# Kernel tuning notes

Measured on AMD Instinct MI355X. Metric: run time of the kernel, lower is better.

## Reference

```python
import jax, jax.numpy as jnp
import numpy as np
from jax import lax

V, H, B, S, NSLOT, T, G, NSW = 20000, 400, 16, 256, 30, 10, 3, 40


def setup_inputs() -> dict:
    key = jax.random.key(0)
    ks = jax.random.split(key, 24)
    p = lambda k, shape: jax.random.normal(k, shape, dtype=jnp.float32) * 0.1
    return {
        'story': jax.random.randint(ks[0], (B, S), 0, V),
        'enc_lens': jax.random.randint(ks[1], (B,), S // 2, S + 1),
        'target_batches': jax.random.randint(ks[2], (B, NSLOT, T), 0, V),
        'domain_idx': jax.random.randint(ks[3], (NSLOT,), 0, NSW),
        'slot_idx': jax.random.randint(ks[4], (NSLOT,), 0, NSW),
        'emb': p(ks[5], (V, H)),
        'enc_Wih_f': p(ks[6], (3 * H, H)), 'enc_Whh_f': p(ks[7], (3 * H, H)),
        'enc_bih_f': p(ks[8], (3 * H,)), 'enc_bhh_f': p(ks[9], (3 * H,)),
        'enc_Wih_b': p(ks[10], (3 * H, H)), 'enc_Whh_b': p(ks[11], (3 * H, H)),
        'enc_bih_b': p(ks[12], (3 * H,)), 'enc_bhh_b': p(ks[13], (3 * H,)),
        'dec_Wih': p(ks[14], (3 * H, H)), 'dec_Whh': p(ks[15], (3 * H, H)),
        'dec_bih': p(ks[16], (3 * H,)), 'dec_bhh': p(ks[17], (3 * H,)),
        'Wr': p(ks[18], (1, 3 * H)), 'br': p(ks[19], (1,)),
        'Wg': p(ks[20], (G, H)), 'bg': p(ks[21], (G,)),
        'slot_table': p(ks[22], (NSW, H)),
    }


def _gru_scan(x, m, h0, Wih, Whh, bih, bhh):
    # x: [S,B,H], m: [S,B] validity mask (packed-sequence semantics)
    def step(h, xm):
        xt, mt = xm
        gi = xt @ Wih.T + bih
        gh = h @ Whh.T + bhh
        ir, iz, inn = jnp.split(gi, 3, -1)
        hr, hz, hn = jnp.split(gh, 3, -1)
        r = jax.nn.sigmoid(ir + hr)
        z = jax.nn.sigmoid(iz + hz)
        n = jnp.tanh(inn + r * hn)
        hnew = (1.0 - z) * n + z * h
        h = jnp.where(mt[:, None], hnew, h)
        y = jnp.where(mt[:, None], hnew, 0.0)
        return h, y
    hT, ys = lax.scan(step, h0, (x, m))
    return ys, hT


def reference(story, enc_lens, target_batches, domain_idx, slot_idx, emb,
              enc_Wih_f, enc_Whh_f, enc_bih_f, enc_bhh_f,
              enc_Wih_b, enc_Whh_b, enc_bih_b, enc_bhh_b,
              dec_Wih, dec_Whh, dec_bih, dec_bhh,
              Wr, br, Wg, bg, slot_table):
    Bc, Sc = story.shape
    nslot = domain_idx.shape[0]
    Tc = target_batches.shape[2]
    NB = nslot * Bc

    # ----- EncoderRNN: bidirectional GRU over story (seq-major) -----
    x = emb[story.T]                                   # [S,B,H]
    mask = jnp.arange(Sc)[:, None] < enc_lens[None, :]  # [S,B]
    h0 = jnp.zeros((Bc, H), jnp.float32)
    ys_f, h_f = _gru_scan(x, mask, h0, enc_Wih_f, enc_Whh_f, enc_bih_f, enc_bhh_f)
    ys_b, h_b = _gru_scan(x[::-1], mask[::-1], h0, enc_Wih_b, enc_Whh_b, enc_bih_b, enc_bhh_b)
    ys_b = ys_b[::-1]
    encoded_outputs = (ys_f + ys_b).transpose(1, 0, 2)  # [B,S,H]
    enc_hidden = h_f + h_b                              # [B,H]

    # ----- Generator (parallel decode, teacher forcing) -----
    combined = slot_table[domain_idx] + slot_table[slot_idx]           # [nslot,H]
    slot_emb_arr = jnp.repeat(combined[:, None, :], Bc, axis=1).reshape(NB, H)
    hidden0 = jnp.tile(enc_hidden, (nslot, 1))                         # [NB,H]
    enc_out = jnp.tile(encoded_outputs, (nslot, 1, 1))                 # [NB,S,H]
    lens_rep = jnp.tile(enc_lens, nslot)
    story_rep = jnp.tile(story, (nslot, 1))                            # [NB,S]
    attn_mask = jnp.arange(Sc)[None, :] < lens_rep[:, None]            # [NB,S]
    rows = jnp.arange(NB)[:, None]

    # teacher-forced decoder inputs: step0 = slot emb, then gold tokens
    tgt_flat = target_batches.transpose(1, 0, 2).reshape(NB, Tc)       # [NB,T]
    dec_in = jnp.concatenate([slot_emb_arr[None], emb[tgt_flat[:, :Tc - 1].T]], axis=0)  # [T,NB,H]

    def dec_step(h, x_in):
        gi = x_in @ dec_Wih.T + dec_bih
        gh = h @ dec_Whh.T + dec_bhh
        ir, iz, inn = jnp.split(gi, 3, -1)
        hr, hz, hn = jnp.split(gh, 3, -1)
        r = jax.nn.sigmoid(ir + hr)
        z = jax.nn.sigmoid(iz + hz)
        n = jnp.tanh(inn + r * hn)
        h = (1.0 - z) * n + z * h                      # dec_state == new hidden
        scores = jnp.einsum('nh,nsh->ns', h, enc_out)
        scores = jnp.where(attn_mask, scores, -jnp.inf)
        prob = jax.nn.softmax(scores, axis=1)          # [NB,S]
        context = jnp.einsum('ns,nsh->nh', prob, enc_out)
        p_vocab = jax.nn.softmax(h @ emb.T, axis=1)    # [NB,V]
        p_gen_vec = jnp.concatenate([h, context, x_in], axis=-1)
        sw = jax.nn.sigmoid(p_gen_vec @ Wr.T + br)     # [NB,1]
        p_ctx = jnp.zeros_like(p_vocab).at[rows, story_rep].add(prob)
        final_p = (1.0 - sw) * p_ctx + sw * p_vocab
        return h, (final_p, context)

    _, (finals, contexts) = lax.scan(dec_step, hidden0, dec_in)
    all_point_outputs = finals.reshape(Tc, nslot, Bc, V).transpose(1, 2, 0, 3)  # [nslot,B,T,V]
    all_gate_outputs = (contexts[0] @ Wg.T + bg).reshape(nslot, Bc, G)
    return all_point_outputs, all_gate_outputs
```

## Files before the change

kernel.cpp:

```cpp
#include <hip/hip_runtime.h>
#include <hip/hip_bf16.h>

typedef unsigned short u16;
typedef __attribute__((ext_vector_type(8))) short bf16x8;
typedef __attribute__((ext_vector_type(4))) float f32x4;
typedef __attribute__((ext_vector_type(4))) unsigned u32x4;

static constexpr int V = 20000, H = 400, B = 16, S = 256, NSLOT = 30, T = 10, G = 3;
static constexpr int H3 = 3 * H;
static constexpr int NB = NSLOT * B;
static constexpr int ENBLK = 20;
static constexpr int ESL   = 20;
static constexpr int EROWS = 64;
static constexpr int EKP   = 416;
static constexpr int HP2 = 424;
static constexpr int SCP = 260;
static constexpr int PP  = 264;
static constexpr int CXP = 404;
static constexpr int FUSED_LDS = 32*HP2*2 + 32*SCP*4 + 32*PP*2 + 32*CXP*4;

__device__ __forceinline__ float bf2f(u16 v) {
    union { unsigned u; float f; } x; x.u = ((unsigned)v) << 16; return x.f;
}
__device__ __forceinline__ u16 f2bf(float f) {
    union { float f; unsigned u; } x; x.f = f;
    unsigned r = x.u + 0x7fffu + ((x.u >> 16) & 1u);
    return (u16)(r >> 16);
}
__device__ __forceinline__ float sigm(float v) { return 1.f / (1.f + __expf(-v)); }

__global__ __launch_bounds__(256) void gemm_bt(
    const u16* __restrict__ A, const u16* __restrict__ Bt,
    const float* __restrict__ bias, float* __restrict__ C,
    int M, int N, int K, int lda, int ldb, long long ldc,
    long long sA, long long sB, long long sC,
    int mode, float* __restrict__ rowsum)
{
    __shared__ u16 As[64][40];
    __shared__ u16 Bs[64][40];
    const int bz = blockIdx.z;
    A  += (long long)bz * sA;
    Bt += (long long)bz * sB;
    C  += (long long)bz * sC;
    const int m0 = blockIdx.x * 64, n0 = blockIdx.y * 64;
    const int tid = threadIdx.x, wave = tid >> 6, lane = tid & 63;
    const int wm = (wave >> 1) * 32, wn = (wave & 1) * 32;
    const int srow = tid >> 2, scol = (tid & 3) * 8;
// ... 77 lines not shown
                float s = acc[i][0][r] + acc[i][1][r];
                s += __shfl_xor(s, 1); s += __shfl_xor(s, 2);
                s += __shfl_xor(s, 4); s += __shfl_xor(s, 8);
                if (fr == 0) {
                    int row = m0 + wm + i * 16 + kq * 4 + r;
                    if (row < M) atomicAdd(&rowsum[row], s);
                }
            }
    }
}

__global__ void cvt_bf16_kernel(const float* __restrict__ src, u16* __restrict__ dst, int n) {
    for (int i = blockIdx.x * blockDim.x + threadIdx.x; i < n; i += gridDim.x * blockDim.x)
        dst[i] = f2bf(src[i]);
}

__global__ void cvt4_kernel(const float* __restrict__ a, const float* __restrict__ b,
                            const float* __restrict__ c, const float* __restrict__ d,
                            u16* __restrict__ da, u16* __restrict__ db,
                            u16* __restrict__ dc, u16* __restrict__ dd, int n) {
    for (int i = blockIdx.x * blockDim.x + threadIdx.x; i < n; i += gridDim.x * blockDim.x) {
        da[i] = f2bf(a[i]); db[i] = f2bf(b[i]); dc[i] = f2bf(c[i]); dd[i] = f2bf(d[i]);
    }
}

__global__ void prep_wenc_kernel(const float* __restrict__ whhf, const float* __restrict__ whhb,
                                 u16* __restrict__ dst) {
    int idx = blockIdx.x * 256 + threadIdx.x;
    const int total = 2 * ENBLK * EROWS * EKP;
    if (idx >= total) return;
    int k = idx % EKP; int r = idx / EKP;
    int rloc = r % EROWS; r /= EROWS;
    int j = r % ENBLK; int dir = r / ENBLK;
    u16 v = 0;
    if (k < H && rloc < 3 * ESL) {
        int g = rloc / ESL, c = rloc % ESL;
        const float* W = dir ? whhb : whhf;
        v = f2bf(W[(long long)(g * H + j * ESL + c) * H + k]);
    }
    dst[idx] = v;
}

__global__ void embed_story_kernel(const int* __restrict__ story, const u16* __restrict__ embb,
                                   u16* __restrict__ xb) {
    int row = blockIdx.x;
    int s = row >> 4, b = row & 15;
    int tok = story[b * S + s];
    const u16* e = embb + (long long)tok * H;
    u16* d = xb + (long long)row * H;
    for (int k = threadIdx.x; k < H; k += blockDim.x) d[k] = e[k];
}

__global__ void build_decin_kernel(const int* __restrict__ tgt, const int* __restrict__ dom,
                                   const int* __restrict__ sidx, const float* __restrict__ slt,
                                   const u16* __restrict__ embb, u16* __restrict__ decin) {
    int n = blockIdx.x, t = blockIdx.y;
    int b = n & 15, slot = n >> 4;
    u16* d = decin + ((long long)t * NB + n) * H;
    if (t == 0) {
        const float* s1 = slt + (long long)dom[slot] * H;
        const float* s2 = slt + (long long)sidx[slot] * H;
        for (int k = threadIdx.x; k < H; k += blockDim.x) d[k] = f2bf(s1[k] + s2[k]);
    } else {
        int tok = tgt[(b * NSLOT + slot) * T + (t - 1)];
        const u16* e = embb + (long long)tok * H;
        for (int k = threadIdx.x; k < H; k += blockDim.x) d[k] = e[k];
    }
}

__global__ __launch_bounds__(256) void enc_rnn2_kernel(
    const u16* __restrict__ wencp,
    const float* __restrict__ bhhf, const float* __restrict__ bhhb,
    const float* __restrict__ gif, const float* __restrict__ gib,
    const int* __restrict__ lens,
    unsigned* __restrict__ hbuf, int* __restrict__ flags,
    float* __restrict__ ysf, float* __restrict__ ysb,
    float* __restrict__ hfo, float* __restrict__ hbo)
{
    const int bid = blockIdx.x;
    const int dir = bid / ENBLK, j = bid % ENBLK;
    const float* bhh = dir ? bhhb : bhhf;
    const float* gi  = dir ? gib  : gif;
    float* ys = dir ? ysb : ysf;
    float* ho = dir ? hbo : hfo;

    __shared__ u16 wlds[EROWS * EKP];
    __shared__ float ghs[EROWS * 17];

    const int tid = threadIdx.x, wave = tid >> 6, lane = tid & 63;
    const int fr = lane & 15, kq = lane >> 4;

    const u16* wsrc = wencp + (long long)(dir * ENBLK + j) * EROWS * EKP;
    for (int i = tid * 8; i < EROWS * EKP; i += 256 * 8)
        *(bf16x8*)&wlds[i] = *(const bf16x8*)&wsrc[i];
    for (int i = tid; i < EROWS * 17; i += 256) ghs[i] = 0.f;

    const int p0 = tid, p1 = 256 + tid;
    const bool has1 = (tid < 64);
    const int b0 = p0 / ESL, kl0 = p0 % ESL;
    const int b1 = has1 ? p1 / ESL : 0, kl1 = has1 ? p1 % ESL : 0;
    const int k0 = j * ESL;
    const int len0 = lens[b0];
    const int len1 = has1 ? lens[b1] : 0;
    const float bhr0 = bhh[k0 + kl0], bhz0 = bhh[H + k0 + kl0], bhn0 = bhh[2 * H + k0 + kl0];
    const float bhr1 = has1 ? bhh[k0 + kl1] : 0.f;
    const float bhz1 = has1 ? bhh[H + k0 + kl1] : 0.f;
    const float bhn1 = has1 ? bhh[2 * H + k0 + kl1] : 0.f;
    float h0r = 0.f, h1r = 0.f;

    unsigned* hb_d = hbuf + (long long)dir * S * B * EKP;
    int* flg_d = flags + dir * S * ENBLK;
    const u16* arow = &wlds[(wave * 16 + fr) * EKP + kq * 8];
    __syncthreads();

    for (int t = 0; t < S; ++t) {
        const int s = dir ? (S - 1 - t) : t;
        const float* gbase = gi + (long long)s * B * H3;
        float gr0 = gbase[b0 * H3 + k0 + kl0];
        float gz0 = gbase[b0 * H3 + H + k0 + kl0];
        float gn0 = gbase[b0 * H3 + 2 * H + k0 + kl0];
        float gr1 = 0.f, gz1 = 0.f, gn1 = 0.f;
        if (has1) {
            gr1 = gbase[b1 * H3 + k0 + kl1];
            gz1 = gbase[b1 * H3 + H + k0 + kl1];
            gn1 = gbase[b1 * H3 + 2 * H + k0 + kl1];
        }

        f32x4 acc = (f32x4){0.f, 0.f, 0.f, 0.f};
        if (t > 0) {
            const int* fl = flg_d + (t - 1) * ENBLK;
            for (;;) {
                int v = 1;
                if (lane < ENBLK)
                    v = __hip_atomic_load(&fl[lane], __ATOMIC_RELAXED,
                                          __HIP_MEMORY_SCOPE_AGENT);
                if (__all(v != 0)) break;
                __builtin_amdgcn_s_sleep(2);
            }
            asm volatile("" ::: "memory");
            const unsigned* hrow = hb_d + ((long long)(t - 1) * B + fr) * EKP + kq * 8;
            f32x4 acch = (f32x4){0.f, 0.f, 0.f, 0.f};
            f32x4 accl = (f32x4){0.f, 0.f, 0.f, 0.f};
#pragma unroll
            for (int kk = 0; kk < 13; ++kk) {
                u32x4 a = *(const u32x4*)(hrow + kk * 32);
                u32x4 b = *(const u32x4*)(hrow + kk * 32 + 4);
                union { unsigned u[4]; bf16x8 v; } hi, lo;
                hi.u[0] = __builtin_amdgcn_perm(a[1], a[0], 0x05040100u);
                hi.u[1] = __builtin_amdgcn_perm(a[3], a[2], 0x05040100u);
                hi.u[2] = __builtin_amdgcn_perm(b[1], b[0], 0x05040100u);
                hi.u[3] = __builtin_amdgcn_perm(b[3], b[2], 0x05040100u);
                lo.u[0] = __builtin_amdgcn_perm(a[1], a[0], 0x07060302u);
                lo.u[1] = __builtin_amdgcn_perm(a[3], a[2], 0x07060302u);
                lo.u[2] = __builtin_amdgcn_perm(b[1], b[0], 0x07060302u);
                lo.u[3] = __builtin_amdgcn_perm(b[3], b[2], 0x07060302u);
                bf16x8 av = *(const bf16x8*)(arow + kk * 32);
                acch = __builtin_amdgcn_mfma_f32_16x16x32_bf16(av, hi.v, acch, 0, 0, 0);
                accl = __builtin_amdgcn_mfma_f32_16x16x32_bf16(av, lo.v, accl, 0, 0, 0);
            }
            acc = acch + accl;
        }
#pragma unroll
        for (int r = 0; r < 4; ++r) ghs[(wave * 16 + kq * 4 + r) * 17 + fr] = acc[r];
        __syncthreads();

        unsigned* hpub = hb_d + (long long)t * B * EKP;
        {
            float ghr = ghs[kl0 * 17 + b0];
            float ghz = ghs[(ESL + kl0) * 17 + b0];
            float ghn = ghs[(2 * ESL + kl0) * 17 + b0];
            float rg = sigm(gr0 + ghr + bhr0);
            float zg = sigm(gz0 + ghz + bhz0);
            float ng = tanhf(gn0 + rg * (ghn + bhn0));
            float hn = (1.f - zg) * ng + zg * h0r;
            bool msk = s < len0;
            float y = msk ? hn : 0.f;
            if (msk) h0r = hn;
            ys[((long long)(b0 * S + s)) * H + k0 + kl0] = y;
            u16 hi = f2bf(h0r);
            unsigned packed = (unsigned)hi | ((unsigned)f2bf(h0r - bf2f(hi)) << 16);
            __hip_atomic_store(&hpub[b0 * EKP + k0 + kl0], packed, __ATOMIC_RELAXED,
                               __HIP_MEMORY_SCOPE_AGENT);
        }
        if (has1) {
            float ghr = ghs[kl1 * 17 + b1];
            float ghz = ghs[(ESL + kl1) * 17 + b1];
            float ghn = ghs[(2 * ESL + kl1) * 17 + b1];
            float rg = sigm(gr1 + ghr + bhr1);
            float zg = sigm(gz1 + ghz + bhz1);
            float ng = tanhf(gn1 + rg * (ghn + bhn1));
            float hn = (1.f - zg) * ng + zg * h1r;
            bool msk = s < len1;
            float y = msk ? hn : 0.f;
            if (msk) h1r = hn;
            ys[((long long)(b1 * S + s)) * H + k0 + kl1] = y;
            u16 hi = f2bf(h1r);
            unsigned packed = (unsigned)hi | ((unsigned)f2bf(h1r - bf2f(hi)) << 16);
            __hip_atomic_store(&hpub[b1 * EKP + k0 + kl1], packed, __ATOMIC_RELAXED,
                               __HIP_MEMORY_SCOPE_AGENT);
        }
        __syncthreads();
        if (tid == 0)
            __hip_atomic_store(&flg_d[t * ENBLK + j], 1, __ATOMIC_RELAXED,
                               __HIP_MEMORY_SCOPE_AGENT);
    }
    ho[b0 * H + k0 + kl0] = h0r;
    if (has1) ho[b1 * H + k0 + kl1] = h1r;
}

__global__ void packE_kernel(const float* __restrict__ ysf, const float* __restrict__ ysb,
                             u16* __restrict__ E, u16* __restrict__ ET) {
    __shared__ u16 tile[32][400];
    const int b = blockIdx.x, s0 = blockIdx.y * 32;
    for (int si = 0; si < 32; ++si) {
        const long long base = ((long long)b * S + s0 + si) * H;
        for (int k = threadIdx.x; k < H; k += blockDim.x) {
            u16 v = f2bf(ysf[base + k] + ysb[base + k]);
            E[base + k] = v;
            tile[si][k] = v;
        }
    }
    __syncthreads();
    for (int idx = threadIdx.x; idx < 32 * H; idx += blockDim.x) {
        int k = idx >> 5, si = idx & 31;
        ET[((long long)b * H + k) * S + s0 + si] = tile[si][k];
    }
}

__global__ void h0_kernel(const float* __restrict__ hf, const float* __restrict__ hb,
                          float* __restrict__ hf32, u16* __restrict__ hnk) {
    int n = blockIdx.x, b = n & 15;
    for (int k = threadIdx.x; k < H; k += blockDim.x) {
        float v = hf[b * H + k] + hb[b * H + k];
        hf32[(long long)n * H + k] = v;
        hnk[(long long)n * H + k] = f2bf(v);
    }
}

__global__ __launch_bounds__(512) void fused_step_kernel(
    const float* __restrict__ dgi, const float* __restrict__ dgh,
    float* __restrict__ hf32, u16* __restrict__ hall,
    const u16* __restrict__ decinb,
    const u16* __restrict__ Eb, const u16* __restrict__ ETb,
    const int* __restrict__ lens,
    const float* __restrict__ Wr, const float* __restrict__ br,
    const float* __restrict__ Wg, const float* __restrict__ bg,
    float* __restrict__ probfT, float* __restrict__ swvT,
    float* __restrict__ gout, int t)
{
    extern __shared__ char smem[];
    u16*   hls = (u16*)smem;
    float* scs = (float*)(smem + 32 * HP2 * 2);
    u16*   pls = (u16*)(smem + 32 * HP2 * 2 + 32 * SCP * 4);
    float* cxs = (float*)(smem + 32 * HP2 * 2 + 32 * SCP * 4 + 32 * PP * 2);

    const int b = blockIdx.x;
    const int tid = threadIdx.x, wave = tid >> 6, lane = tid & 63;
    const int fr = lane & 15, kq = lane >> 4;
    const int len = lens[b];

    for (int i = tid; i < 32 * (HP2 - H); i += 512) {
        int r = i / (HP2 - H), c = H + i % (HP2 - H);
        hls[r * HP2 + c] = 0;
    }
    for (int i = tid; i < 2 * HP2; i += 512) hls[30 * HP2 + i] = 0;
    for (int i = tid; i < 2 * PP; i += 512) pls[30 * PP + i] = 0;

    for (int i = tid; i < 30 * H; i += 512) {
        int slot = i / H, k = i % H;
        int n = slot * 16 + b;
        const float* gi = dgi + ((long long)t * NB + n) * H3;
        const float* gh = dgh + (long long)n * H3;
        float r  = sigm(gi[k] + gh[k]);
        float z  = sigm(gi[H + k] + gh[H + k]);
        float nn = tanhf(gi[2 * H + k] + r * gh[2 * H + k]);
        float h  = hf32[(long long)n * H + k];
        float hn = (1.f - z) * nn + z * h;
        hf32[(long long)n * H + k] = hn;
        u16 hb = f2bf(hn);
        hall[((long long)t * NB + n) * H + k] = hb;
        hls[slot * HP2 + k] = hb;
    }
    __syncthreads();

    {
        const int nt0 = wave * 2;
        f32x4 acc[2][2];
#pragma unroll
        for (int i = 0; i < 2; ++i)
#pragma unroll
            for (int jj = 0; jj < 2; ++jj) acc[i][jj] = (f32x4){0.f, 0.f, 0.f, 0.f};
        const u16* br0 = Eb + ((long long)b * S + nt0 * 16 + fr) * H + kq * 8;
        const u16* br1 = Eb + ((long long)b * S + (nt0 + 1) * 16 + fr) * H + kq * 8;
        const u16* ar0 = hls + fr * HP2 + kq * 8;
        const u16* ar1 = hls + (16 + fr) * HP2 + kq * 8;
#pragma unroll
        for (int kk = 0; kk < 13; ++kk) {
            bf16x8 av0 = *(const bf16x8*)(ar0 + kk * 32);
            bf16x8 av1 = *(const bf16x8*)(ar1 + kk * 32);
            bf16x8 bv0, bv1;
            if (kk == 12 && kq >= 2) {
                bv0 = (bf16x8){0,0,0,0,0,0,0,0}; bv1 = bv0;
            } else {
                bv0 = *(const bf16x8*)(br0 + kk * 32);
                bv1 = *(const bf16x8*)(br1 + kk * 32);
            }
            acc[0][0] = __builtin_amdgcn_mfma_f32_16x16x32_bf16(av0, bv0, acc[0][0], 0, 0, 0);
            acc[1][0] = __builtin_amdgcn_mfma_f32_16x16x32_bf16(av1, bv0, acc[1][0], 0, 0, 0);
            acc[0][1] = __builtin_amdgcn_mfma_f32_16x16x32_bf16(av0, bv1, acc[0][1], 0, 0, 0);
            acc[1][1] = __builtin_amdgcn_mfma_f32_16x16x32_bf16(av1, bv1, acc[1][1], 0, 0, 0);
        }
#pragma unroll
        for (int i = 0; i < 2; ++i)
#pragma unroll
            for (int jj = 0; jj < 2; ++jj)
#pragma unroll
                for (int r = 0; r < 4; ++r)
                    scs[(i * 16 + kq * 4 + r) * SCP + (nt0 + jj) * 16 + fr] = acc[i][jj][r];
    }
    __syncthreads();

    for (int i = 0; i < 4; ++i) {
        int row = wave * 4 + i;
        if (row >= 30) break;
        int n = row * 16 + b;
        float v[4];
        float mx = -3.0e38f;
#pragma unroll
        for (int q = 0; q < 4; ++q) {
            int s = lane + 64 * q;
            float x = (s < len) ? scs[row * SCP + s] : -3.0e38f;
            v[q] = x; mx = fmaxf(mx, x);
        }
        mx = fmaxf(mx, __shfl_xor(mx, 1));  mx = fmaxf(mx, __shfl_xor(mx, 2));
        mx = fmaxf(mx, __shfl_xor(mx, 4));  mx = fmaxf(mx, __shfl_xor(mx, 8));
        mx = fmaxf(mx, __shfl_xor(mx, 16)); mx = fmaxf(mx, __shfl_xor(mx, 32));
        float sum = 0.f;
#pragma unroll
        for (int q = 0; q < 4; ++q) {
            int s = lane + 64 * q;
            float e = (s < len) ? __expf(v[q] - mx) : 0.f;
            v[q] = e; sum += e;
        }
        sum += __shfl_xor(sum, 1);  sum += __shfl_xor(sum, 2);
        sum += __shfl_xor(sum, 4);  sum += __shfl_xor(sum, 8);
        sum += __shfl_xor(sum, 16); sum += __shfl_xor(sum, 32);
        float inv = 1.f / sum;
#pragma unroll
        for (int q = 0; q < 4; ++q) {
            int s = lane + 64 * q;
            float pr = v[q] * inv;
            pls[row * PP + s] = f2bf(pr);
            probfT[((long long)(t * NB + n)) * S + s] = pr;
        }
    }
    __syncthreads();

    for (int nt = wave; nt < 25; nt += 8) {
        f32x4 acc0 = (f32x4){0.f,0.f,0.f,0.f}, acc1 = (f32x4){0.f,0.f,0.f,0.f};
        const u16* brow = ETb + ((long long)b * H + nt * 16 + fr) * S + kq * 8;
        const u16* ar0 = pls + fr * PP + kq * 8;
        const u16* ar1 = pls + (16 + fr) * PP + kq * 8;
#pragma unroll
        for (int kk = 0; kk < 8; ++kk) {
            bf16x8 bv  = *(const bf16x8*)(brow + kk * 32);
            bf16x8 av0 = *(const bf16x8*)(ar0 + kk * 32);
            bf16x8 av1 = *(const bf16x8*)(ar1 + kk * 32);
            acc0 = __builtin_amdgcn_mfma_f32_16x16x32_bf16(av0, bv, acc0, 0, 0, 0);
            acc1 = __builtin_amdgcn_mfma_f32_16x16x32_bf16(av1, bv, acc1, 0, 0, 0);
        }
#pragma unroll
        for (int r = 0; r < 4; ++r) {
            cxs[(kq * 4 + r) * CXP + nt * 16 + fr] = acc0[r];
            cxs[(16 + kq * 4 + r) * CXP + nt * 16 + fr] = acc1[r];
        }
    }
    __syncthreads();

    for (int i = 0; i < 4; ++i) {
        int slot = wave + 8 * i;
        if (slot >= 30) break;
        int n = slot * 16 + b;
        const u16* xrow = decinb + ((long long)t * NB + n) * H;
        float p = 0.f;
        for (int k = lane; k < H; k += 64)
            p += bf2f(hls[slot * HP2 + k]) * Wr[k]
               + cxs[slot * CXP + k] * Wr[H + k]
               + bf2f(xrow[k]) * Wr[2 * H + k];
        p += __shfl_xor(p, 1);  p += __shfl_xor(p, 2);
        p += __shfl_xor(p, 4);  p += __shfl_xor(p, 8);
        p += __shfl_xor(p, 16); p += __shfl_xor(p, 32);
        if (lane == 0) swvT[t * NB + n] = sigm(p + br[0]);
        if (t == 0) {
            for (int g = 0; g < G; ++g) {
                float q = 0.f;
                for (int k = lane; k < H; k += 64)
                    q += cxs[slot * CXP + k] * Wg[g * H + k];
                q += __shfl_xor(q, 1);  q += __shfl_xor(q, 2);
                q += __shfl_xor(q, 4);  q += __shfl_xor(q, 8);
                q += __shfl_xor(q, 16); q += __shfl_xor(q, 32);
                if (lane == 0) gout[(long long)n * G + g] = q + bg[g];
            }
        }
    }
}

__global__ void scale_all_kernel(float* __restrict__ out, const float* __restrict__ swvT,
                                 const float* __restrict__ rowsumT) {
    const int n = blockIdx.x;
    const int col = blockIdx.y * 256 + threadIdx.x;
    if (col >= V) return;
#pragma unroll
    for (int t = 0; t < T; ++t) {
        float f = swvT[t * NB + n] / rowsumT[t * NB + n];
        out[((long long)n * T + t) * V + col] *= f;
    }
}

__global__ void scatter_all_kernel(float* __restrict__ out, const int* __restrict__ story,
                                   const int* __restrict__ lens, const float* __restrict__ swvT,
                                   const float* __restrict__ probfT) {
    const int n = blockIdx.x, t = blockIdx.y, b = n & 15, s = threadIdx.x;
    if (s < lens[b]) {
        int tok = story[b * S + s];
        atomicAdd(out + ((long long)n * T + t) * V + tok,
                  (1.f - swvT[t * NB + n]) * probfT[((long long)(t * NB + n)) * S + s]);
    }
}

extern "C" void kernel_launch(void* const* d_in, const int* in_sizes, int n_in,
                              void* d_out, int out_size, void* d_ws, size_t ws_size,
                              hipStream_t stream) {
    const int*   story = (const int*)d_in[0];
    const int*   lens  = (const int*)d_in[1];
    const int*   tgt   = (const int*)d_in[2];
    const int*   dom   = (const int*)d_in[3];
// ... 2 lines not shown
    const float* wihf  = (const float*)d_in[6];
    const float* whhf  = (const float*)d_in[7];
    const float* bihf  = (const float*)d_in[8];
    const float* bhhf  = (const float*)d_in[9];
    const float* wihb  = (const float*)d_in[10];
    const float* whhb  = (const float*)d_in[11];
    const float* bihb  = (const float*)d_in[12];
    const float* bhhb  = (const float*)d_in[13];
    const float* dwih  = (const float*)d_in[14];
    const float* dwhh  = (const float*)d_in[15];
    const float* dbih  = (const float*)d_in[16];
    const float* dbhh  = (const float*)d_in[17];
    const float* Wr    = (const float*)d_in[18];
    const float* br    = (const float*)d_in[19];
    const float* Wg    = (const float*)d_in[20];
    const float* bg    = (const float*)d_in[21];
    const float* slt   = (const float*)d_in[22];
    float* out = (float*)d_out;

    char* wsb = (char*)d_ws;
    size_t off = 0;
    auto alloc = [&](size_t bytes) -> char* {
        char* p = wsb + off;
        off += (bytes + 255) & ~(size_t)255;
        return p;
    };
    u16*   embb   = (u16*)alloc((size_t)V * H * 2);
    u16*   wihfb  = (u16*)alloc((size_t)H3 * H * 2);
    u16*   wihbb  = (u16*)alloc((size_t)H3 * H * 2);
    u16*   dwihb  = (u16*)alloc((size_t)H3 * H * 2);
    u16*   dwhhb  = (u16*)alloc((size_t)H3 * H * 2);
    u16*   wencp  = (u16*)alloc((size_t)2 * ENBLK * EROWS * EKP * 2);
    unsigned* hbuf = (unsigned*)alloc((size_t)2 * S * B * EKP * 4);
    int*   flags  = (int*)alloc((size_t)2 * S * ENBLK * 4);
    u16*   xb     = (u16*)alloc((size_t)S * B * H * 2);
    u16*   decinb = (u16*)alloc((size_t)T * NB * H * 2);
    float* gif    = (float*)alloc((size_t)S * B * H3 * 4);
    float* gib    = (float*)alloc((size_t)S * B * H3 * 4);
    float* dgi    = (float*)alloc((size_t)T * NB * H3 * 4);
    float* ysf    = (float*)alloc((size_t)B * S * H * 4);
    float* ysb    = (float*)alloc((size_t)B * S * H * 4);
    float* hfv    = (float*)alloc((size_t)B * H * 4);
    float* hbv    = (float*)alloc((size_t)B * H * 4);
    u16*   Eb     = (u16*)alloc((size_t)B * S * H * 2);
    u16*   ETb    = (u16*)alloc((size_t)B * H * S * 2);
    float* hf32   = (float*)alloc((size_t)NB * H * 4);
    u16*   hnk    = (u16*)alloc((size_t)NB * H * 2);
    u16*   hall   = (u16*)alloc((size_t)T * NB * H * 2);
    float* dgh    = (float*)alloc((size_t)NB * H3 * 4);
    float* probfT = (float*)alloc((size_t)T * NB * S * 4);
    float* swvT   = (float*)alloc((size_t)T * NB * 4);
    float* rowsumT = (float*)alloc((size_t)T * NB * 4);
    (void)ws_size; (void)in_sizes; (void)n_in; (void)out_size;

    auto launch_gemm = [&](const u16* A, const u16* Bt, const float* bias, float* C,
                           int M, int N, int K, int lda, int ldb, long long ldc,
                           long long sA, long long sB, long long sC, int nb,
                           int mode, float* rs) {
        dim3 g((M + 63) / 64, (N + 63) / 64, nb);
        gemm_bt<<<g, 256, 0, stream>>>(A, Bt, bias, C, M, N, K, lda, ldb, ldc,
                                       sA, sB, sC, mode, rs);
    };

    hipFuncSetAttribute((const void*)fused_step_kernel,
                        hipFuncAttributeMaxDynamicSharedMemorySize, FUSED_LDS);

    cvt_bf16_kernel<<<2048, 256, 0, stream>>>(emb, embb, V * H);
    cvt4_kernel<<<1024, 256, 0, stream>>>(wihf, wihb, dwih, dwhh,
                                          wihfb, wihbb, dwihb, dwhhb, H3 * H);
    {
        const int total = 2 * ENBLK * EROWS * EKP;
        prep_wenc_kernel<<<(total + 255) / 256, 256, 0, stream>>>(whhf, whhb, wencp);
    }
    embed_story_kernel<<<S * B, 256, 0, stream>>>(story, embb, xb);
    { dim3 g(NB, T); build_decin_kernel<<<g, 256, 0, stream>>>(tgt, dom, sidx, slt, embb, decinb); }

    launch_gemm(xb, wihfb, bihf, gif, S * B, H3, H, H, H, H3, 0, 0, 0, 1, 0, nullptr);
    launch_gemm(xb, wihbb, bihb, gib, S * B, H3, H, H, H, H3, 0, 0, 0, 1, 0, nullptr);
    launch_gemm(decinb, dwihb, dbih, dgi, T * NB, H3, H, H, H, H3, 0, 0, 0, 1, 0, nullptr);

    hipMemsetAsync(flags, 0, (size_t)2 * S * ENBLK * 4, stream);
    hipMemsetAsync(hbuf, 0, (size_t)2 * S * B * EKP * 4, stream);
    hipMemsetAsync(rowsumT, 0, (size_t)T * NB * 4, stream);
    enc_rnn2_kernel<<<2 * ENBLK, 256, 0, stream>>>(wencp, bhhf, bhhb, gif, gib, lens,
                                                   hbuf, flags, ysf, ysb, hfv, hbv);
    { dim3 g(B, S / 32); packE_kernel<<<g, 256, 0, stream>>>(ysf, ysb, Eb, ETb); }
    h0_kernel<<<NB, 256, 0, stream>>>(hfv, hbv, hf32, hnk);

    for (int t = 0; t < T; ++t) {
        const u16* hprev = (t == 0) ? hnk : hall + (size_t)(t - 1) * NB * H;
        launch_gemm(hprev, dwhhb, dbhh, dgh, NB, H3, H, H, H, H3, 0, 0, 0, 1, 0, nullptr);
        fused_step_kernel<<<16, 512, FUSED_LDS, stream>>>(
            dgi, dgh, hf32, hall, decinb, Eb, ETb, lens, Wr, br, Wg, bg,
            probfT, swvT, out + (size_t)NB * T * V, t);
    }

    launch_gemm(hall, embb, nullptr, out, T * NB, V, H, H, H, V,
                0, 0, 0, 1, 2, rowsumT);
    { dim3 g(NB, (V + 255) / 256); scale_all_kernel<<<g, 256, 0, stream>>>(out, swvT, rowsumT); }
    { dim3 g(NB, T); scatter_all_kernel<<<g, 256, 0, stream>>>(out, story, lens, swvT, probfT); }
}
```

Before: 2.473 ms.

## Make encoder GRU waves independent with per-wave flags instead of block barriers

```diff
diff --git a/kernel.cpp b/kernel.cpp
--- a/kernel.cpp
+++ b/kernel.cpp
@@ -13,6 +13,7 @@
 static constexpr int ESL   = 20;
 static constexpr int EROWS = 64;
 static constexpr int EKP   = 416;
+static constexpr int NFLG  = 4 * ENBLK;
 static constexpr int HP2 = 424;
 static constexpr int SCP = 260;
 static constexpr int PP  = 264;
@@ -156,11 +157,12 @@
     int k = idx % EKP; int r = idx / EKP;
     int rloc = r % EROWS; r /= EROWS;
     int j = r % ENBLK; int dir = r / ENBLK;
+    int w = rloc >> 4, m = rloc & 15;
     u16 v = 0;
-    if (k < H && rloc < 3 * ESL) {
-        int g = rloc / ESL, c = rloc % ESL;
+    if (k < H && m < 15) {
+        int g = m / 5, cc = m % 5;
         const float* W = dir ? whhb : whhf;
-        v = f2bf(W[(long long)(g * H + j * ESL + c) * H + k]);
+        v = f2bf(W[(long long)(g * H + j * ESL + w * 5 + cc) * H + k]);
     }
     dst[idx] = v;
 }
@@ -192,7 +194,7 @@
     }
 }
 
-__global__ __launch_bounds__(256) void enc_rnn2_kernel(
+__global__ __launch_bounds__(256) void enc_rnn_bf_kernel(
     const u16* __restrict__ wencp,
     const float* __restrict__ bhhf, const float* __restrict__ bhhb,
     const float* __restrict__ gif, const float* __restrict__ gib,
@@ -209,56 +211,53 @@
     float* ho = dir ? hbo : hfo;
 
     __shared__ u16 wlds[EROWS * EKP];
-    __shared__ float ghs[EROWS * 17];
-
-    const int tid = threadIdx.x, wave = tid >> 6, lane = tid & 63;
+    __shared__ float ghs[4][16 * 17];
+
+    const int tid = threadIdx.x, w = tid >> 6, lane = tid & 63;
     const int fr = lane & 15, kq = lane >> 4;
 
     const u16* wsrc = wencp + (long long)(dir * ENBLK + j) * EROWS * EKP;
-    for (int i = tid * 8; i < EROWS * EKP; i += 256 * 8)
-        *(bf16x8*)&wlds[i] = *(const bf16x8*)&wsrc[i];
-    for (int i = tid; i < EROWS * 17; i += 256) ghs[i] = 0.f;
-
-    const int p0 = tid, p1 = 256 + tid;
-    const bool has1 = (tid < 64);
-    const int b0 = p0 / ESL, kl0 = p0 % ESL;
-    const int b1 = has1 ? p1 / ESL : 0, kl1 = has1 ? p1 % ESL : 0;
-    const int k0 = j * ESL;
-    const int len0 = lens[b0];
-    const int len1 = has1 ? lens[b1] : 0;
-    const float bhr0 = bhh[k0 + kl0], bhz0 = bhh[H + k0 + kl0], bhn0 = bhh[2 * H + k0 + kl0];
-    const float bhr1 = has1 ? bhh[k0 + kl1] : 0.f;
-    const float bhz1 = has1 ? bhh[H + k0 + kl1] : 0.f;
-    const float bhn1 = has1 ? bhh[2 * H + k0 + kl1] : 0.f;
+    for (int i = lane * 8; i < 16 * EKP; i += 64 * 8)
+        *(bf16x8*)&wlds[w * 16 * EKP + i] = *(const bf16x8*)&wsrc[w * 16 * EKP + i];
+
+    const int b = fr;
+    const int k0g = j * ESL + w * 5 + kq;
+    const bool has1 = (kq == 0);
+    const int k1g = j * ESL + w * 5 + 4;
+    const int len = lens[b];
+    const float bhr0 = bhh[k0g], bhz0 = bhh[H + k0g], bhn0 = bhh[2 * H + k0g];
+    const float bhr1 = has1 ? bhh[k1g] : 0.f;
+    const float bhz1 = has1 ? bhh[H + k1g] : 0.f;
+    const float bhn1 = has1 ? bhh[2 * H + k1g] : 0.f;
     float h0r = 0.f, h1r = 0.f;
 
     unsigned* hb_d = hbuf + (long long)dir * S * B * EKP;
-    int* flg_d = flags + dir * S * ENBLK;
-    const u16* arow = &wlds[(wave * 16 + fr) * EKP + kq * 8];
-    __syncthreads();
+    int* flg_d = flags + dir * S * NFLG;
+    const u16* arow = &wlds[(w * 16 + fr) * EKP + kq * 8];
+    float* ghw = ghs[w];
 
     for (int t = 0; t < S; ++t) {
         const int s = dir ? (S - 1 - t) : t;
         const float* gbase = gi + (long long)s * B * H3;
-        float gr0 = gbase[b0 * H3 + k0 + kl0];
-        float gz0 = gbase[b0 * H3 + H + k0 + kl0];
-        float gn0 = gbase[b0 * H3 + 2 * H + k0 + kl0];
+        float gr0 = gbase[b * H3 + k0g];
+        float gz0 = gbase[b * H3 + H + k0g];
+        float gn0 = gbase[b * H3 + 2 * H + k0g];
         float gr1 = 0.f, gz1 = 0.f, gn1 = 0.f;
         if (has1) {
-            gr1 = gbase[b1 * H3 + k0 + kl1];
-            gz1 = gbase[b1 * H3 + H + k0 + kl1];
-            gn1 = gbase[b1 * H3 + 2 * H + k0 + kl1];
+            gr1 = gbase[b * H3 + k1g];
+            gz1 = gbase[b * H3 + H + k1g];
+            gn1 = gbase[b * H3 + 2 * H + k1g];
         }
 
         f32x4 acc = (f32x4){0.f, 0.f, 0.f, 0.f};
         if (t > 0) {
-            const int* fl = flg_d + (t - 1) * ENBLK;
+            const int* fl = flg_d + (t - 1) * NFLG;
             for (;;) {
-                int v = 1;
-                if (lane < ENBLK)
-                    v = __hip_atomic_load(&fl[lane], __ATOMIC_RELAXED,
-                                          __HIP_MEMORY_SCOPE_AGENT);
-                if (__all(v != 0)) break;
+                int v1 = __hip_atomic_load(&fl[lane], __ATOMIC_RELAXED,
+                                           __HIP_MEMORY_SCOPE_AGENT);
+                int v2 = __hip_atomic_load(&fl[16 + lane], __ATOMIC_RELAXED,
+                                           __HIP_MEMORY_SCOPE_AGENT);
+                if (__all(v1 != 0 && v2 != 0)) break;
                 __builtin_amdgcn_s_sleep(2);
             }
             asm volatile("" ::: "memory");
@@ -268,16 +267,16 @@
 #pragma unroll
             for (int kk = 0; kk < 13; ++kk) {
                 u32x4 a = *(const u32x4*)(hrow + kk * 32);
-                u32x4 b = *(const u32x4*)(hrow + kk * 32 + 4);
+                u32x4 c = *(const u32x4*)(hrow + kk * 32 + 4);
                 union { unsigned u[4]; bf16x8 v; } hi, lo;
                 hi.u[0] = __builtin_amdgcn_perm(a[1], a[0], 0x05040100u);
                 hi.u[1] = __builtin_amdgcn_perm(a[3], a[2], 0x05040100u);
-                hi.u[2] = __builtin_amdgcn_perm(b[1], b[0], 0x05040100u);
-                hi.u[3] = __builtin_amdgcn_perm(b[3], b[2], 0x05040100u);
+                hi.u[2] = __builtin_amdgcn_perm(c[1], c[0], 0x05040100u);
+                hi.u[3] = __builtin_amdgcn_perm(c[3], c[2], 0x05040100u);
                 lo.u[0] = __builtin_amdgcn_perm(a[1], a[0], 0x07060302u);
                 lo.u[1] = __builtin_amdgcn_perm(a[3], a[2], 0x07060302u);
-                lo.u[2] = __builtin_amdgcn_perm(b[1], b[0], 0x07060302u);
-                lo.u[3] = __builtin_amdgcn_perm(b[3], b[2], 0x07060302u);
+                lo.u[2] = __builtin_amdgcn_perm(c[1], c[0], 0x07060302u);
+                lo.u[3] = __builtin_amdgcn_perm(c[3], c[2], 0x07060302u);
                 bf16x8 av = *(const bf16x8*)(arow + kk * 32);
                 acch = __builtin_amdgcn_mfma_f32_16x16x32_bf16(av, hi.v, acch, 0, 0, 0);
                 accl = __builtin_amdgcn_mfma_f32_16x16x32_bf16(av, lo.v, accl, 0, 0, 0);
@@ -285,51 +284,51 @@
             acc = acch + accl;
         }
 #pragma unroll
-        for (int r = 0; r < 4; ++r) ghs[(wave * 16 + kq * 4 + r) * 17 + fr] = acc[r];
-        __syncthreads();
+        for (int r = 0; r < 4; ++r) ghw[(kq * 4 + r) * 17 + fr] = acc[r];
+        __builtin_amdgcn_wave_barrier();
 
         unsigned* hpub = hb_d + (long long)t * B * EKP;
         {
-            float ghr = ghs[kl0 * 17 + b0];
-            float ghz = ghs[(ESL + kl0) * 17 + b0];
-            float ghn = ghs[(2 * ESL + kl0) * 17 + b0];
+            float ghr = ghw[kq * 17 + b];
+            float ghz = ghw[(5 + kq) * 17 + b];
+            float ghn = ghw[(10 + kq) * 17 + b];
             float rg = sigm(gr0 + ghr + bhr0);
             float zg = sigm(gz0 + ghz + bhz0);
             float ng = tanhf(gn0 + rg * (ghn + bhn0));
             float hn = (1.f - zg) * ng + zg * h0r;
-            bool msk = s < len0;
+            bool msk = s < len;
             float y = msk ? hn : 0.f;
             if (msk) h0r = hn;
-            ys[((long long)(b0 * S + s)) * H + k0 + kl0] = y;
+            ys[((long long)(b * S + s)) * H + k0g] = y;
             u16 hi = f2bf(h0r);
             unsigned packed = (unsigned)hi | ((unsigned)f2bf(h0r - bf2f(hi)) << 16);
-            __hip_atomic_store(&hpub[b0 * EKP + k0 + kl0], packed, __ATOMIC_RELAXED,
+            __hip_atomic_store(&hpub[b * EKP + k0g], packed, __ATOMIC_RELAXED,
                                __HIP_MEMORY_SCOPE_AGENT);
         }
         if (has1) {
-            float ghr = ghs[kl1 * 17 + b1];
-            float ghz = ghs[(ESL + kl1) * 17 + b1];
-            float ghn = ghs[(2 * ESL + kl1) * 17 + b1];
+            float ghr = ghw[4 * 17 + b];
+            float ghz = ghw[9 * 17 + b];
+            float ghn = ghw[14 * 17 + b];
             float rg = sigm(gr1 + ghr + bhr1);
             float zg = sigm(gz1 + ghz + bhz1);
             float ng = tanhf(gn1 + rg * (ghn + bhn1));
             float hn = (1.f - zg) * ng + zg * h1r;
-            bool msk = s < len1;
+            bool msk = s < len;
             float y = msk ? hn : 0.f;
             if (msk) h1r = hn;
-            ys[((long long)(b1 * S + s)) * H + k0 + kl1] = y;
+            ys[((long long)(b * S + s)) * H + k1g] = y;
             u16 hi = f2bf(h1r);
             unsigned packed = (unsigned)hi | ((unsigned)f2bf(h1r - bf2f(hi)) << 16);
-            __hip_atomic_store(&hpub[b1 * EKP + k0 + kl1], packed, __ATOMIC_RELAXED,
+            __hip_atomic_store(&hpub[b * EKP + k1g], packed, __ATOMIC_RELAXED,
                                __HIP_MEMORY_SCOPE_AGENT);
         }
-        __syncthreads();
-        if (tid == 0)
-            __hip_atomic_store(&flg_d[t * ENBLK + j], 1, __ATOMIC_RELAXED,
+        asm volatile("s_waitcnt vmcnt(0)" ::: "memory");
+        if (lane == 0)
+            __hip_atomic_store(&flg_d[t * NFLG + j * 4 + w], 1, __ATOMIC_RELAXED,
                                __HIP_MEMORY_SCOPE_AGENT);
     }
-    ho[b0 * H + k0 + kl0] = h0r;
-    if (has1) ho[b1 * H + k0 + kl1] = h1r;
+    ho[b * H + k0g] = h0r;
+    if (has1) ho[b * H + k1g] = h1r;
 }
 
 __global__ void packE_kernel(const float* __restrict__ ysf, const float* __restrict__ ysb,
@@ -594,7 +593,7 @@
     u16*   dwhhb  = (u16*)alloc((size_t)H3 * H * 2);
     u16*   wencp  = (u16*)alloc((size_t)2 * ENBLK * EROWS * EKP * 2);
     unsigned* hbuf = (unsigned*)alloc((size_t)2 * S * B * EKP * 4);
-    int*   flags  = (int*)alloc((size_t)2 * S * ENBLK * 4);
+    int*   flags  = (int*)alloc((size_t)2 * S * NFLG * 4);
     u16*   xb     = (u16*)alloc((size_t)S * B * H * 2);
     u16*   decinb = (u16*)alloc((size_t)T * NB * H * 2);
     float* gif    = (float*)alloc((size_t)S * B * H3 * 4);
@@ -641,11 +640,11 @@
     launch_gemm(xb, wihbb, bihb, gib, S * B, H3, H, H, H, H3, 0, 0, 0, 1, 0, nullptr);
     launch_gemm(decinb, dwihb, dbih, dgi, T * NB, H3, H, H, H, H3, 0, 0, 0, 1, 0, nullptr);
 
-    hipMemsetAsync(flags, 0, (size_t)2 * S * ENBLK * 4, stream);
+    hipMemsetAsync(flags, 0, (size_t)2 * S * NFLG * 4, stream);
     hipMemsetAsync(hbuf, 0, (size_t)2 * S * B * EKP * 4, stream);
     hipMemsetAsync(rowsumT, 0, (size_t)T * NB * 4, stream);
-    enc_rnn2_kernel<<<2 * ENBLK, 256, 0, stream>>>(wencp, bhhf, bhhb, gif, gib, lens,
-                                                   hbuf, flags, ysf, ysb, hfv, hbv);
+    enc_rnn_bf_kernel<<<2 * ENBLK, 256, 0, stream>>>(wencp, bhhf, bhhb, gif, gib, lens,
+                                                     hbuf, flags, ysf, ysb, hfv, hbv);
     { dim3 g(B, S / 32); packE_kernel<<<g, 256, 0, stream>>>(ysf, ysb, Eb, ETb); }
     h0_kernel<<<NB, 256, 0, stream>>>(hfv, hbv, hf32, hnk);
 
```

Result: slower. 3.136 ms (+26.8%).

## Fuse decoder recurrence into one persistent kernel with in-block Whh GEMM

Applied to the files above, without the earlier changes.

```diff
diff --git a/kernel.cpp b/kernel.cpp
--- a/kernel.cpp
+++ b/kernel.cpp
@@ -351,35 +351,27 @@
     }
 }
 
-__global__ void h0_kernel(const float* __restrict__ hf, const float* __restrict__ hb,
-                          float* __restrict__ hf32, u16* __restrict__ hnk) {
-    int n = blockIdx.x, b = n & 15;
-    for (int k = threadIdx.x; k < H; k += blockDim.x) {
-        float v = hf[b * H + k] + hb[b * H + k];
-        hf32[(long long)n * H + k] = v;
-        hnk[(long long)n * H + k] = f2bf(v);
-    }
-}
-
-__global__ __launch_bounds__(512) void fused_step_kernel(
-    const float* __restrict__ dgi, const float* __restrict__ dgh,
-    float* __restrict__ hf32, u16* __restrict__ hall,
-    const u16* __restrict__ decinb,
+__global__ __launch_bounds__(512) void decoder_persist_kernel(
+    const float* __restrict__ dgi, const u16* __restrict__ dwhhb,
+    const float* __restrict__ dbhh,
+    const float* __restrict__ hfv, const float* __restrict__ hbv,
+    u16* __restrict__ hall, const u16* __restrict__ decinb,
     const u16* __restrict__ Eb, const u16* __restrict__ ETb,
     const int* __restrict__ lens,
     const float* __restrict__ Wr, const float* __restrict__ br,
     const float* __restrict__ Wg, const float* __restrict__ bg,
     float* __restrict__ probfT, float* __restrict__ swvT,
-    float* __restrict__ gout, int t)
+    float* __restrict__ gout)
 {
     extern __shared__ char smem[];
     u16*   hls = (u16*)smem;
     float* scs = (float*)(smem + 32 * HP2 * 2);
     u16*   pls = (u16*)(smem + 32 * HP2 * 2 + 32 * SCP * 4);
     float* cxs = (float*)(smem + 32 * HP2 * 2 + 32 * SCP * 4 + 32 * PP * 2);
+    u16* scs_h = (u16*)scs;
 
     const int b = blockIdx.x;
-    const int tid = threadIdx.x, wave = tid >> 6, lane = tid & 63;
+    const int tid = threadIdx.x, w = tid >> 6, lane = tid & 63;
     const int fr = lane & 15, kq = lane >> 4;
     const int len = lens[b];
 
@@ -392,140 +384,199 @@
 
     for (int i = tid; i < 30 * H; i += 512) {
         int slot = i / H, k = i % H;
-        int n = slot * 16 + b;
-        const float* gi = dgi + ((long long)t * NB + n) * H3;
-        const float* gh = dgh + (long long)n * H3;
-        float r  = sigm(gi[k] + gh[k]);
-        float z  = sigm(gi[H + k] + gh[H + k]);
-        float nn = tanhf(gi[2 * H + k] + r * gh[2 * H + k]);
-        float h  = hf32[(long long)n * H + k];
-        float hn = (1.f - z) * nn + z * h;
-        hf32[(long long)n * H + k] = hn;
-        u16 hb = f2bf(hn);
-        hall[((long long)t * NB + n) * H + k] = hb;
-        hls[slot * HP2 + k] = hb;
+        hls[slot * HP2 + k] = f2bf(hfv[b * H + k] + hbv[b * H + k]);
+    }
+    float hreg[4][2][4];
+    float bhr[4], bhz[4], bhn[4];
+#pragma unroll
+    for (int q = 0; q < 4; ++q) {
+        int kc = w + 8 * q;
+        if (kc < 25) {
+            int c = kc * 16 + fr;
+            float h0 = hfv[b * H + c] + hbv[b * H + c];
+            bhr[q] = dbhh[c]; bhz[q] = dbhh[H + c]; bhn[q] = dbhh[2 * H + c];
+#pragma unroll
+            for (int i = 0; i < 2; ++i)
+#pragma unroll
+                for (int r = 0; r < 4; ++r) hreg[q][i][r] = h0;
+        }
     }
     __syncthreads();
 
-    {
-        const int nt0 = wave * 2;
-        f32x4 acc[2][2];
-#pragma unroll
-        for (int i = 0; i < 2; ++i)
-#pragma unroll
-            for (int jj = 0; jj < 2; ++jj) acc[i][jj] = (f32x4){0.f, 0.f, 0.f, 0.f};
-        const u16* br0 = Eb + ((long long)b * S + nt0 * 16 + fr) * H + kq * 8;
-        const u16* br1 = Eb + ((long long)b * S + (nt0 + 1) * 16 + fr) * H + kq * 8;
-        const u16* ar0 = hls + fr * HP2 + kq * 8;
-        const u16* ar1 = hls + (16 + fr) * HP2 + kq * 8;
-#pragma unroll
-        for (int kk = 0; kk < 13; ++kk) {
-            bf16x8 av0 = *(const bf16x8*)(ar0 + kk * 32);
-            bf16x8 av1 = *(const bf16x8*)(ar1 + kk * 32);
-            bf16x8 bv0, bv1;
-            if (kk == 12 && kq >= 2) {
-                bv0 = (bf16x8){0,0,0,0,0,0,0,0}; bv1 = bv0;
-            } else {
-                bv0 = *(const bf16x8*)(br0 + kk * 32);
-                bv1 = *(const bf16x8*)(br1 + kk * 32);
-            }
-            acc[0][0] = __builtin_amdgcn_mfma_f32_16x16x32_bf16(av0, bv0, acc[0][0], 0, 0, 0);
-            acc[1][0] = __builtin_amdgcn_mfma_f32_16x16x32_bf16(av1, bv0, acc[1][0], 0, 0, 0);
-            acc[0][1] = __builtin_amdgcn_mfma_f32_16x16x32_bf16(av0, bv1, acc[0][1], 0, 0, 0);
-            acc[1][1] = __builtin_amdgcn_mfma_f32_16x16x32_bf16(av1, bv1, acc[1][1], 0, 0, 0);
-        }
-#pragma unroll
-        for (int i = 0; i < 2; ++i)
-#pragma unroll
-            for (int jj = 0; jj < 2; ++jj)
-#pragma unroll
-                for (int r = 0; r < 4; ++r)
-                    scs[(i * 16 + kq * 4 + r) * SCP + (nt0 + jj) * 16 + fr] = acc[i][jj][r];
-    }
-    __syncthreads();
-
-    for (int i = 0; i < 4; ++i) {
-        int row = wave * 4 + i;
-        if (row >= 30) break;
-        int n = row * 16 + b;
-        float v[4];
-        float mx = -3.0e38f;
+    for (int t = 0; t < T; ++t) {
 #pragma unroll
         for (int q = 0; q < 4; ++q) {
-            int s = lane + 64 * q;
-            float x = (s < len) ? scs[row * SCP + s] : -3.0e38f;
-            v[q] = x; mx = fmaxf(mx, x);
-        }
-        mx = fmaxf(mx, __shfl_xor(mx, 1));  mx = fmaxf(mx, __shfl_xor(mx, 2));
-        mx = fmaxf(mx, __shfl_xor(mx, 4));  mx = fmaxf(mx, __shfl_xor(mx, 8));
-        mx = fmaxf(mx, __shfl_xor(mx, 16)); mx = fmaxf(mx, __shfl_xor(mx, 32));
-        float sum = 0.f;
-#pragma unroll
-        for (int q = 0; q < 4; ++q) {
-            int s = lane + 64 * q;
-            float e = (s < len) ? __expf(v[q] - mx) : 0.f;
-            v[q] = e; sum += e;
-        }
-        sum += __shfl_xor(sum, 1);  sum += __shfl_xor(sum, 2);
-        sum += __shfl_xor(sum, 4);  sum += __shfl_xor(sum, 8);
-        sum += __shfl_xor(sum, 16); sum += __shfl_xor(sum, 32);
-        float inv = 1.f / sum;
-#pragma unroll
-        for (int q = 0; q < 4; ++q) {
-            int s = lane + 64 * q;
-            float pr = v[q] * inv;
-            pls[row * PP + s] = f2bf(pr);
-            probfT[((long long)(t * NB + n)) * S + s] = pr;
-        }
-    }
-    __syncthreads();
-
-    for (int nt = wave; nt < 25; nt += 8) {
-        f32x4 acc0 = (f32x4){0.f,0.f,0.f,0.f}, acc1 = (f32x4){0.f,0.f,0.f,0.f};
-        const u16* brow = ETb + ((long long)b * H + nt * 16 + fr) * S + kq * 8;
-        const u16* ar0 = pls + fr * PP + kq * 8;
-        const u16* ar1 = pls + (16 + fr) * PP + kq * 8;
-#pragma unroll
-        for (int kk = 0; kk < 8; ++kk) {
-            bf16x8 bv  = *(const bf16x8*)(brow + kk * 32);
-            bf16x8 av0 = *(const bf16x8*)(ar0 + kk * 32);
-            bf16x8 av1 = *(const bf16x8*)(ar1 + kk * 32);
-            acc0 = __builtin_amdgcn_mfma_f32_16x16x32_bf16(av0, bv, acc0, 0, 0, 0);
-            acc1 = __builtin_amdgcn_mfma_f32_16x16x32_bf16(av1, bv, acc1, 0, 0, 0);
-        }
-#pragma unroll
-        for (int r = 0; r < 4; ++r) {
-            cxs[(kq * 4 + r) * CXP + nt * 16 + fr] = acc0[r];
-            cxs[(16 + kq * 4 + r) * CXP + nt * 16 + fr] = acc1[r];
-        }
-    }
-    __syncthreads();
-
-    for (int i = 0; i < 4; ++i) {
-        int slot = wave + 8 * i;
-        if (slot >= 30) break;
-        int n = slot * 16 + b;
-        const u16* xrow = decinb + ((long long)t * NB + n) * H;
-        float p = 0.f;
-        for (int k = lane; k < H; k += 64)
-            p += bf2f(hls[slot * HP2 + k]) * Wr[k]
-               + cxs[slot * CXP + k] * Wr[H + k]
-               + bf2f(xrow[k]) * Wr[2 * H + k];
-        p += __shfl_xor(p, 1);  p += __shfl_xor(p, 2);
-        p += __shfl_xor(p, 4);  p += __shfl_xor(p, 8);
-        p += __shfl_xor(p, 16); p += __shfl_xor(p, 32);
-        if (lane == 0) swvT[t * NB + n] = sigm(p + br[0]);
-        if (t == 0) {
-            for (int g = 0; g < G; ++g) {
-                float q = 0.f;
-                for (int k = lane; k < H; k += 64)
-                    q += cxs[slot * CXP + k] * Wg[g * H + k];
-                q += __shfl_xor(q, 1);  q += __shfl_xor(q, 2);
-                q += __shfl_xor(q, 4);  q += __shfl_xor(q, 8);
-                q += __shfl_xor(q, 16); q += __shfl_xor(q, 32);
-                if (lane == 0) gout[(long long)n * G + g] = q + bg[g];
-            }
-        }
+            int kc = w + 8 * q;
+            if (kc >= 25) continue;
+            const int cb = kc * 16;
+            const int c = cb + fr;
+            f32x4 gacc[3][2];
+#pragma unroll
+            for (int g = 0; g < 3; ++g)
+#pragma unroll
+                for (int i = 0; i < 2; ++i) gacc[g][i] = (f32x4){0.f, 0.f, 0.f, 0.f};
+#pragma unroll
+            for (int g = 0; g < 3; ++g) {
+                const u16* brow = dwhhb + (long long)(g * H + cb + fr) * H + kq * 8;
+                const u16* ar0 = hls + fr * HP2 + kq * 8;
+                const u16* ar1 = hls + (16 + fr) * HP2 + kq * 8;
+#pragma unroll
+                for (int kk = 0; kk < 13; ++kk) {
+                    bf16x8 bv;
+                    if (kk == 12 && kq >= 2) bv = (bf16x8){0,0,0,0,0,0,0,0};
+                    else bv = *(const bf16x8*)(brow + kk * 32);
+                    bf16x8 av0 = *(const bf16x8*)(ar0 + kk * 32);
+                    bf16x8 av1 = *(const bf16x8*)(ar1 + kk * 32);
+                    gacc[g][0] = __builtin_amdgcn_mfma_f32_16x16x32_bf16(av0, bv, gacc[g][0], 0, 0, 0);
+                    gacc[g][1] = __builtin_amdgcn_mfma_f32_16x16x32_bf16(av1, bv, gacc[g][1], 0, 0, 0);
+                }
+            }
+            const float* gbase = dgi + ((long long)t * NB + b) * H3;
+#pragma unroll
+            for (int i = 0; i < 2; ++i)
+#pragma unroll
+                for (int r = 0; r < 4; ++r) {
+                    int slotr = i * 16 + kq * 4 + r;
+                    if (slotr >= 30) continue;
+                    const float* gir = gbase + (long long)slotr * 16 * H3;
+                    float rg = sigm(gir[c] + gacc[0][i][r] + bhr[q]);
+                    float zg = sigm(gir[H + c] + gacc[1][i][r] + bhz[q]);
+                    float ng = tanhf(gir[2 * H + c] + rg * (gacc[2][i][r] + bhn[q]));
+                    float hn = (1.f - zg) * ng + zg * hreg[q][i][r];
+                    hreg[q][i][r] = hn;
+                    scs_h[slotr * 400 + c] = f2bf(hn);
+                }
+        }
+        __syncthreads();
+        for (int i = tid; i < 30 * H; i += 512) {
+            int slot = i / H, k = i % H;
+            u16 v = scs_h[i];
+            hls[slot * HP2 + k] = v;
+            hall[((long long)t * NB + slot * 16 + b) * H + k] = v;
+        }
+        __syncthreads();
+
+        {
+            const int nt0 = w * 2;
+            f32x4 acc[2][2];
+#pragma unroll
+            for (int i = 0; i < 2; ++i)
+#pragma unroll
+                for (int jj = 0; jj < 2; ++jj) acc[i][jj] = (f32x4){0.f, 0.f, 0.f, 0.f};
+            const u16* br0 = Eb + ((long long)b * S + nt0 * 16 + fr) * H + kq * 8;
+            const u16* br1 = Eb + ((long long)b * S + (nt0 + 1) * 16 + fr) * H + kq * 8;
+            const u16* ar0 = hls + fr * HP2 + kq * 8;
+            const u16* ar1 = hls + (16 + fr) * HP2 + kq * 8;
+#pragma unroll
+            for (int kk = 0; kk < 13; ++kk) {
+                bf16x8 av0 = *(const bf16x8*)(ar0 + kk * 32);
+                bf16x8 av1 = *(const bf16x8*)(ar1 + kk * 32);
+                bf16x8 bv0, bv1;
+                if (kk == 12 && kq >= 2) {
+                    bv0 = (bf16x8){0,0,0,0,0,0,0,0}; bv1 = bv0;
+                } else {
+                    bv0 = *(const bf16x8*)(br0 + kk * 32);
+                    bv1 = *(const bf16x8*)(br1 + kk * 32);
+                }
+                acc[0][0] = __builtin_amdgcn_mfma_f32_16x16x32_bf16(av0, bv0, acc[0][0], 0, 0, 0);
+                acc[1][0] = __builtin_amdgcn_mfma_f32_16x16x32_bf16(av1, bv0, acc[1][0], 0, 0, 0);
+                acc[0][1] = __builtin_amdgcn_mfma_f32_16x16x32_bf16(av0, bv1, acc[0][1], 0, 0, 0);
+                acc[1][1] = __builtin_amdgcn_mfma_f32_16x16x32_bf16(av1, bv1, acc[1][1], 0, 0, 0);
+            }
+#pragma unroll
+            for (int i = 0; i < 2; ++i)
+#pragma unroll
+                for (int jj = 0; jj < 2; ++jj)
+#pragma unroll
+                    for (int r = 0; r < 4; ++r)
+                        scs[(i * 16 + kq * 4 + r) * SCP + (nt0 + jj) * 16 + fr] = acc[i][jj][r];
+        }
+        __syncthreads();
+
+        for (int i = 0; i < 4; ++i) {
+            int row = w * 4 + i;
+            if (row >= 30) break;
+            int n = row * 16 + b;
+            float v[4];
+            float mx = -3.0e38f;
+#pragma unroll
+            for (int q = 0; q < 4; ++q) {
+                int s = lane + 64 * q;
+                float x = (s < len) ? scs[row * SCP + s] : -3.0e38f;
+                v[q] = x; mx = fmaxf(mx, x);
+            }
+            mx = fmaxf(mx, __shfl_xor(mx, 1));  mx = fmaxf(mx, __shfl_xor(mx, 2));
+            mx = fmaxf(mx, __shfl_xor(mx, 4));  mx = fmaxf(mx, __shfl_xor(mx, 8));
+            mx = fmaxf(mx, __shfl_xor(mx, 16)); mx = fmaxf(mx, __shfl_xor(mx, 32));
+            float sum = 0.f;
+#pragma unroll
+            for (int q = 0; q < 4; ++q) {
+                int s = lane + 64 * q;
+                float e = (s < len) ? __expf(v[q] - mx) : 0.f;
+                v[q] = e; sum += e;
+            }
+            sum += __shfl_xor(sum, 1);  sum += __shfl_xor(sum, 2);
+            sum += __shfl_xor(sum, 4);  sum += __shfl_xor(sum, 8);
+            sum += __shfl_xor(sum, 16); sum += __shfl_xor(sum, 32);
+            float inv = 1.f / sum;
+#pragma unroll
+            for (int q = 0; q < 4; ++q) {
+                int s = lane + 64 * q;
+                float pr = v[q] * inv;
+                pls[row * PP + s] = f2bf(pr);
+                probfT[((long long)(t * NB + n)) * S + s] = pr;
+            }
+        }
+        __syncthreads();
+
+        for (int nt = w; nt < 25; nt += 8) {
+            f32x4 acc0 = (f32x4){0.f,0.f,0.f,0.f}, acc1 = (f32x4){0.f,0.f,0.f,0.f};
+            const u16* brow = ETb + ((long long)b * H + nt * 16 + fr) * S + kq * 8;
+            const u16* ar0 = pls + fr * PP + kq * 8;
+            const u16* ar1 = pls + (16 + fr) * PP + kq * 8;
+#pragma unroll
+            for (int kk = 0; kk < 8; ++kk) {
+                bf16x8 bv  = *(const bf16x8*)(brow + kk * 32);
+                bf16x8 av0 = *(const bf16x8*)(ar0 + kk * 32);
+                bf16x8 av1 = *(const bf16x8*)(ar1 + kk * 32);
+                acc0 = __builtin_amdgcn_mfma_f32_16x16x32_bf16(av0, bv, acc0, 0, 0, 0);
+                acc1 = __builtin_amdgcn_mfma_f32_16x16x32_bf16(av1, bv, acc1, 0, 0, 0);
+            }
+#pragma unroll
+            for (int r = 0; r < 4; ++r) {
+                cxs[(kq * 4 + r) * CXP + nt * 16 + fr] = acc0[r];
+                cxs[(16 + kq * 4 + r) * CXP + nt * 16 + fr] = acc1[r];
+            }
+        }
+        __syncthreads();
+
+        for (int i = 0; i < 4; ++i) {
+            int slot = w + 8 * i;
+            if (slot >= 30) break;
+            int n = slot * 16 + b;
+            const u16* xrow = decinb + ((long long)t * NB + n) * H;
+            float p = 0.f;
+            for (int k = lane; k < H; k += 64)
+                p += bf2f(hls[slot * HP2 + k]) * Wr[k]
+                   + cxs[slot * CXP + k] * Wr[H + k]
+                   + bf2f(xrow[k]) * Wr[2 * H + k];
+            p += __shfl_xor(p, 1);  p += __shfl_xor(p, 2);
+            p += __shfl_xor(p, 4);  p += __shfl_xor(p, 8);
+            p += __shfl_xor(p, 16); p += __shfl_xor(p, 32);
+            if (lane == 0) swvT[t * NB + n] = sigm(p + br[0]);
+            if (t == 0) {
+                for (int g = 0; g < G; ++g) {
+                    float qv = 0.f;
+                    for (int k = lane; k < H; k += 64)
+                        qv += cxs[slot * CXP + k] * Wg[g * H + k];
+                    qv += __shfl_xor(qv, 1);  qv += __shfl_xor(qv, 2);
+                    qv += __shfl_xor(qv, 4);  qv += __shfl_xor(qv, 8);
+                    qv += __shfl_xor(qv, 16); qv += __shfl_xor(qv, 32);
+                    if (lane == 0) gout[(long long)n * G + g] = qv + bg[g];
+                }
+            }
+        }
+        __syncthreads();
     }
 }
 
@@ -606,10 +657,7 @@
     float* hbv    = (float*)alloc((size_t)B * H * 4);
     u16*   Eb     = (u16*)alloc((size_t)B * S * H * 2);
     u16*   ETb    = (u16*)alloc((size_t)B * H * S * 2);
-    float* hf32   = (float*)alloc((size_t)NB * H * 4);
-    u16*   hnk    = (u16*)alloc((size_t)NB * H * 2);
     u16*   hall   = (u16*)alloc((size_t)T * NB * H * 2);
-    float* dgh    = (float*)alloc((size_t)NB * H3 * 4);
     float* probfT = (float*)alloc((size_t)T * NB * S * 4);
     float* swvT   = (float*)alloc((size_t)T * NB * 4);
     float* rowsumT = (float*)alloc((size_t)T * NB * 4);
@@ -624,7 +672,7 @@
                                        sA, sB, sC, mode, rs);
     };
 
-    hipFuncSetAttribute((const void*)fused_step_kernel,
+    hipFuncSetAttribute((const void*)decoder_persist_kernel,
                         hipFuncAttributeMaxDynamicSharedMemorySize, FUSED_LDS);
 
     cvt_bf16_kernel<<<2048, 256, 0, stream>>>(emb, embb, V * H);
@@ -647,15 +695,10 @@
     enc_rnn2_kernel<<<2 * ENBLK, 256, 0, stream>>>(wencp, bhhf, bhhb, gif, gib, lens,
                                                    hbuf, flags, ysf, ysb, hfv, hbv);
     { dim3 g(B, S / 32); packE_kernel<<<g, 256, 0, stream>>>(ysf, ysb, Eb, ETb); }
-    h0_kernel<<<NB, 256, 0, stream>>>(hfv, hbv, hf32, hnk);
-
-    for (int t = 0; t < T; ++t) {
-        const u16* hprev = (t == 0) ? hnk : hall + (size_t)(t - 1) * NB * H;
-        launch_gemm(hprev, dwhhb, dbhh, dgh, NB, H3, H, H, H, H3, 0, 0, 0, 1, 0, nullptr);
-        fused_step_kernel<<<16, 512, FUSED_LDS, stream>>>(
-            dgi, dgh, hf32, hall, decinb, Eb, ETb, lens, Wr, br, Wg, bg,
-            probfT, swvT, out + (size_t)NB * T * V, t);
-    }
+
+    decoder_persist_kernel<<<16, 512, FUSED_LDS, stream>>>(
+        dgi, dwhhb, dbhh, hfv, hbv, hall, decinb, Eb, ETb, lens,
+        Wr, br, Wg, bg, probfT, swvT, out + (size_t)NB * T * V);
 
     launch_gemm(hall, embb, nullptr, out, T * NB, V, H, H, H, V,
                 0, 0, 0, 1, 2, rowsumT);
```

Result: slower. 2.953 ms (+19.4%).
